# Kernel optimization log

Measured on AMD Instinct MI355X. Metric: run time of the kernel, lower is better.

## Reference

```python
import jax, jax.numpy as jnp
import numpy as np

B, S, H = 1, 2048, 2048
E, I = 16, 1408
I_SHARED = 5632
TOP_K = 2


def setup_inputs() -> dict:
    key = jax.random.key(0)
    ks = jax.random.split(key, 8)
    scale = 0.02
    return {
        "hidden_states": jax.random.normal(ks[0], (B, S, H), dtype=jnp.float32),
        "router_w": jax.random.normal(ks[1], (H, E), dtype=jnp.float32) * scale,
        "expert_gate_up_w": jax.random.normal(ks[2], (E, H, 2 * I), dtype=jnp.float32) * scale,
        "expert_out_w": jax.random.normal(ks[3], (E, I, H), dtype=jnp.float32) * scale,
        "shared_ffw_gate_w": jax.random.normal(ks[4], (H, I_SHARED), dtype=jnp.float32) * scale,
        "shared_ffw_inter_w": jax.random.normal(ks[5], (H, I_SHARED), dtype=jnp.float32) * scale,
        "shared_ffw_out_w": jax.random.normal(ks[6], (I_SHARED, H), dtype=jnp.float32) * scale,
        "shared_gate_w": jax.random.normal(ks[7], (H, 1), dtype=jnp.float32) * scale,
        "top_k": TOP_K,
    }


def reference(hidden_states, router_w, expert_gate_up_w, expert_out_w,
              shared_ffw_gate_w, shared_ffw_inter_w, shared_ffw_out_w,
              shared_gate_w, top_k):
    b, s, h = hidden_states.shape
    e = router_w.shape[-1]
    x = hidden_states.reshape(-1, h)  # [T, H]

    # --- Router: softmax over experts, top-k, renormalize (norm_top_k_prob=True) ---
    router_logits = x @ router_w                        # [T, E]
    router_probs = jax.nn.softmax(router_logits, -1)
    top_p, top_i = jax.lax.top_k(router_probs, top_k)   # [T, K]
    top_p = top_p / jnp.sum(top_p, axis=-1, keepdims=True)
    # dense routing matrix [E, T] (matches one_hot-sum-transpose in source)
    one_hot = jax.nn.one_hot(top_i, e, dtype=top_p.dtype)  # [T, K, E]
    routing_full = jnp.sum(one_hot * top_p[..., None], axis=1).T  # [E, T]

    # --- Dense per-expert SwiGLU over ALL tokens (as in QwenMoeExperts) ---
    gate_up = jnp.einsum('th,ehm->etm', x, expert_gate_up_w)  # [E, T, 2I]
    gate, up = jnp.split(gate_up, 2, axis=-1)
    hidden = up * jax.nn.silu(gate)                           # [E, T, I]
    expert_out = jnp.einsum('eti,eih->eth', hidden, expert_out_w)  # [E, T, H]
    expert_contribution = jnp.einsum('eth,et->th', expert_out, routing_full)

    # --- Shared expert (SwiGLU MLP) with sigmoid gate ---
    sgate = jax.nn.silu(x @ shared_ffw_gate_w)
    sinter = x @ shared_ffw_inter_w
    shared_out = (sinter * sgate) @ shared_ffw_out_w          # [T, H]
    shared_out = shared_out * jax.nn.sigmoid(x @ shared_gate_w)

    out = (expert_contribution + shared_out).reshape(b, s, h)
    return out, router_logits
```

## Files before the change

kernel.cpp:

```cpp
#include <hip/hip_runtime.h>
#include <math.h>

typedef __attribute__((ext_vector_type(4))) float f32x4;
typedef __attribute__((ext_vector_type(2))) unsigned int u32x2;
typedef __attribute__((ext_vector_type(4))) unsigned int u32x4;
typedef __attribute__((ext_vector_type(8))) unsigned short u16x8;
typedef __attribute__((ext_vector_type(8))) __bf16 bf16x8;
typedef unsigned short ushort_t;

#define H_DIM 2048
#define T_TOK 2048
#define NEXP 16
#define I_DIM 1408
#define I2_DIM 2816
#define IS_DIM 5632
#define MAXROWS 6144

static __device__ __forceinline__ unsigned short f2bf(float f){
  union { float f; unsigned u; } v; v.f = f;
  unsigned r = v.u + 0x7FFFu + ((v.u >> 16) & 1u);
  return (unsigned short)(r >> 16);
}
static __device__ __forceinline__ float bf2f(unsigned short h){
  union { unsigned u; float f; } v; v.u = ((unsigned)h) << 16;
  return v.f;
}
static __device__ __forceinline__ float silu_f(float x){ return x / (1.f + __expf(-x)); }

static __device__ __forceinline__ void gld16(const ushort_t* g, ushort_t* l){
  __builtin_amdgcn_global_load_lds(
      (const __attribute__((address_space(1))) unsigned int*)g,
      (__attribute__((address_space(3))) unsigned int*)l, 16, 0, 0);
}
static __device__ __forceinline__ bf16x8 dsr128(unsigned byte_off){
  u32x4 r;
  asm volatile("ds_read_b128 %0, %1" : "=v"(r) : "v"(byte_off));
  return __builtin_bit_cast(bf16x8, r);
}

static __device__ __forceinline__ int swz_r(int nwg, int wgo){
  int q = nwg >> 3, r = nwg & 7;
  int xcd = wgo & 7, idx = wgo >> 3;
  return (xcd < r ? xcd * (q + 1) : r * (q + 1) + (xcd - r) * q) + idx;
}

static __device__ __forceinline__ void tr_tile(const float* __restrict__ in,
                                               ushort_t* __restrict__ out,
                                               int K, int N, int k0, int n0){
  __shared__ float tl[128][65];
  int t = threadIdx.x;
  int lr = t >> 4;
  int lc = t & 15;
  #pragma unroll
  for (int p = 0; p < 8; p++){
    int row = p * 16 + lr;
    f32x4 v = __builtin_nontemporal_load((const f32x4*)&in[(long)(k0 + row) * N + n0 + lc * 4]);
    tl[row][lc*4 + 0] = v[0]; tl[row][lc*4 + 1] = v[1];
    tl[row][lc*4 + 2] = v[2]; tl[row][lc*4 + 3] = v[3];
  }
  __syncthreads();
  #pragma unroll
  for (int p = 0; p < 4; p++){
    int n = p * 16 + lr;
    int kc = lc * 8;
    union { ushort_t s[8]; u32x4 v; } pk;
    #pragma unroll
    for (int j = 0; j < 8; j++) pk.s[j] = f2bf(tl[kc + j][n]);
    __builtin_nontemporal_store(pk.v, (u32x4*)&out[(long)(n0 + n) * K + k0 + kc]);
  }
}

#define TR_O1 11264
#define TR_O2 16896
#define TR_O3 18304
#define TR_O4 19712
#define TR_TOT 21120

__global__ void k_tr_router(const float* __restrict__ x, const float* __restrict__ rw,
                            const float* __restrict__ sgw, float* __restrict__ logits,
                            int* __restrict__ counts, int* __restrict__ lists,
                            float* __restrict__ probs, float* __restrict__ sgmul,
                            ushort_t* __restrict__ xb,
                            const float* __restrict__ wgu, const float* __restrict__ wout,
                            const float* __restrict__ wsg, const float* __restrict__ wsi,
                            const float* __restrict__ wso,
                            ushort_t* __restrict__ wgu_t, ushort_t* __restrict__ wout_t,
                            ushort_t* __restrict__ wsg_t, ushort_t* __restrict__ wsi_t,
                            ushort_t* __restrict__ wso_t){
  int b = blockIdx.x;
  if (b < 512){
    int wid = threadIdx.x >> 6, lane = threadIdx.x & 63;
    int t = b * 4 + wid;
    const float* xr = x + (long)t * H_DIM;
    ushort_t* xbr = xb + (long)t * H_DIM;
    float acc[17];
    #pragma unroll
    for (int e = 0; e < 17; e++) acc[e] = 0.f;
    for (int h0 = lane * 4; h0 < H_DIM; h0 += 256){
      f32x4 xv = *(const f32x4*)&xr[h0];
      u32x2 pk;
      pk[0] = (unsigned)f2bf(xv[0]) | ((unsigned)f2bf(xv[1]) << 16);
      pk[1] = (unsigned)f2bf(xv[2]) | ((unsigned)f2bf(xv[3]) << 16);
      *(u32x2*)&xbr[h0] = pk;
      #pragma unroll
      for (int i = 0; i < 4; i++){
        float xs = xv[i];
        const float* wrow = rw + (long)(h0 + i) * NEXP;
        #pragma unroll
        for (int e = 0; e < 16; e++) acc[e] += xs * wrow[e];
        acc[16] += xs * sgw[h0 + i];
      }
    }
    #pragma unroll
    for (int e = 0; e < 17; e++)
      for (int off = 32; off >= 1; off >>= 1)
        acc[e] += __shfl_xor(acc[e], off);
    if (lane == 0){
      float* lo = logits + (long)t * NEXP;
      #pragma unroll
      for (int e = 0; e < 16; e++) lo[e] = acc[e];
      int e0 = 0;
      #pragma unroll
      for (int e = 1; e < 16; e++) if (acc[e] > acc[e0]) e0 = e;
      int e1 = (e0 == 0) ? 1 : 0;
      #pragma unroll
      for (int e = 0; e < 16; e++) if (e != e0 && acc[e] > acc[e1]) e1 = e;
      float d = acc[e1] - acc[e0];
      float ed = __expf(d);
      float p0 = 1.f / (1.f + ed);
      float p1 = ed / (1.f + ed);
      int pos0 = atomicAdd(&counts[e0], 1);
      lists[e0 * T_TOK + pos0] = t; probs[e0 * T_TOK + pos0] = p0;
      int pos1 = atomicAdd(&counts[e1], 1);
      lists[e1 * T_TOK + pos1] = t; probs[e1 * T_TOK + pos1] = p1;
      sgmul[t] = 1.f / (1.f + __expf(-acc[16]));
    }
    return;
  }
  int bb = b - 512;
  if (bb < TR_O1){
    int e = bb / 704, r = bb % 704;
    int ky = r / 44, nx = r % 44;
    long zo = (long)e * H_DIM * I2_DIM;
    tr_tile(wgu + zo, wgu_t + zo, H_DIM, I2_DIM, ky * 128, nx * 64);
  } else if (bb < TR_O2){
    int r = bb - TR_O1;
    int e = r / 352; r %= 352;
    int ky = r / 32, nx = r % 32;
    long zo = (long)e * I_DIM * H_DIM;
    tr_tile(wout + zo, wout_t + zo, I_DIM, H_DIM, ky * 128, nx * 64);
  } else if (bb < TR_O3){
    int r = bb - TR_O2;
    int ky = r / 88, nx = r % 88;
    tr_tile(wsg, wsg_t, H_DIM, IS_DIM, ky * 128, nx * 64);
  } else if (bb < TR_O4){
    int r = bb - TR_O3;
    int ky = r / 88, nx = r % 88;
    tr_tile(wsi, wsi_t, H_DIM, IS_DIM, ky * 128, nx * 64);
  } else {
    int r = bb - TR_O4;
    int ky = r / 32, nx = r % 32;
    tr_tile(wso, wso_t, IS_DIM, H_DIM, ky * 128, nx * 64);
  }
}

__global__ void bases_k(const int* __restrict__ counts, int* __restrict__ bases){
  if (threadIdx.x == 0){
    int r = 0;
    for (int e = 0; e < NEXP; e++){ bases[e] = r; r += (counts[e] + 127) & ~127; }
  }
}

static __device__ __forceinline__ void gemm_core(
    const ushort_t* __restrict__ Ab, int lda,
    const ushort_t* __restrict__ Bb, int ldbt, int kb,
    int m0, int n0, int cnt, const int* __restrict__ gather, int emode,
    ushort_t* __restrict__ Cb, int ldc, long rbase,
    const int* __restrict__ sclist, const float* __restrict__ scprob,
    const float* __restrict__ svec, float* __restrict__ outp){
  __shared__ ushort_t lds[3 * 8192];
  unsigned lbase = (unsigned)(size_t)(__attribute__((address_space(3))) ushort_t*)lds;

  int tid = threadIdx.x;
  int lane = tid & 63;
  int wv = tid >> 6;
  int wm = wv >> 1;
  int wn = wv & 1;

  int srow = lane >> 2;
  int sslot = ((lane & 3) ^ (srow & 3)) * 8;
  long aoff[2], boff[2];
  #pragma unroll
  for (int c = 0; c < 2; c++){
    int mr = wv * 32 + c * 16 + srow;
    int grow;
    if (gather){
      int j = m0 + mr; if (j >= cnt) j = cnt - 1;
      grow = gather[j];
    } else {
      grow = m0 + mr;
    }
    aoff[c] = (long)grow * lda + sslot;
    boff[c] = (long)(n0 + mr) * ldbt + sslot;
  }

  auto stage = [&](int t, int buf){
    long ko = (long)t * 32;
    ushort_t* dA = lds + buf * 8192 + wv * 1024;
    ushort_t* dB = dA + 4096;
    gld16(Ab + aoff[0] + ko, dA);
    gld16(Ab + aoff[1] + ko, dA + 512);
    gld16(Bb + boff[0] + ko, dB);
    gld16(Bb + boff[1] + ko, dB + 512);
  };

  f32x4 zero = {0.f, 0.f, 0.f, 0.f};
  f32x4 acc[4][4];
  #pragma unroll
  for (int i = 0; i < 4; i++)
    #pragma unroll
    for (int j = 0; j < 4; j++) acc[i][j] = zero;

  int fr = lane & 15;
  int kg = lane >> 4;
  unsigned ps = (unsigned)((kg ^ (fr & 3)) << 4);
  unsigned aoffb = (unsigned)((wm * 64 + fr) * 64) + ps;
  unsigned boffb = 8192u + (unsigned)((wn * 64 + fr) * 64) + ps;

  int nt = kb >> 5;
  stage(0, 0);
  __builtin_amdgcn_sched_barrier(0);
  stage(1, 1);

  int rb = 0, sb = 2;
  for (int t = 0; t < nt; t++){
    if (t + 2 < nt) asm volatile("s_waitcnt vmcnt(4)" ::: "memory");
    else            asm volatile("s_waitcnt vmcnt(0)" ::: "memory");
    __builtin_amdgcn_s_barrier();
    __builtin_amdgcn_sched_barrier(0);
    unsigned bufb = lbase + (unsigned)rb * 16384u;
    bf16x8 af[4], bg[4];
    #pragma unroll
    for (int f = 0; f < 4; f++){
      af[f] = dsr128(bufb + aoffb + f * 1024u);
      bg[f] = dsr128(bufb + boffb + f * 1024u);
    }
    __builtin_amdgcn_sched_barrier(0);
    if (t + 2 < nt) stage(t + 2, sb);
    asm volatile("s_waitcnt lgkmcnt(0)" ::: "memory");
    __builtin_amdgcn_sched_barrier(0);
    #pragma unroll
    for (int fm = 0; fm < 4; fm++)
      #pragma unroll
      for (int fn = 0; fn < 4; fn++)
        acc[fm][fn] = __builtin_amdgcn_mfma_f32_16x16x32_bf16(af[fm], bg[fn], acc[fm][fn], 0, 0, 0);
    rb = (rb == 2) ? 0 : rb + 1;
    sb = (sb == 2) ? 0 : sb + 1;
  }

  int colb = n0 + wn * 64 + (lane & 15);
  int rowb = m0 + wm * 64 + (lane >> 4) * 4;
  #pragma unroll
  for (int fm = 0; fm < 4; fm++){
    #pragma unroll
    for (int fn = 0; fn < 4; fn++){
      f32x4 v = acc[fm][fn];
      int col = colb + fn * 16;
      #pragma unroll
      for (int rr = 0; rr < 4; rr++){
        int m = rowb + fm * 16 + rr;
        if (emode == 0){
          Cb[(long)m * ldc + col] = f2bf(v[rr]);
        } else if (emode == 1){
          if (m < cnt) Cb[(rbase + m) * (long)ldc + col] = f2bf(v[rr]);
        } else if (emode == 2){
          if (m < cnt){
            int tok = sclist[m];
            atomicAdd(outp + (long)tok * ldc + col, scprob[m] * v[rr]);
          }
        } else {
          atomicAdd(outp + (long)m * ldc + col, svec[m] * v[rr]);
        }
      }
    }
  }
}

__global__ __launch_bounds__(256) void g_shared_gi(
    const ushort_t* xb, const ushort_t* wsg_t, const ushort_t* wsi_t, ushort_t* sgr){
  int z = blockIdx.z;
  int wg = swz_r(704, blockIdx.x);
  int m0 = (wg % 16) * 128, n0 = (wg / 16) * 128;
  gemm_core(xb, H_DIM, (z ? wsi_t : wsg_t), H_DIM, H_DIM, m0, n0, T_TOK,
            nullptr, 0, sgr + (size_t)z * T_TOK * IS_DIM, IS_DIM, 0,
            nullptr, nullptr, nullptr, nullptr);
}

__global__ __launch_bounds__(256) void k_gu_flat(
    const ushort_t* xb, const ushort_t* wgu_t, ushort_t* gu,
    const int* counts, const int* bases, const int* lists,
    ushort_t* sg, const ushort_t* si){
  int b = blockIdx.x;
  if (b < 5632){
    int e = b / 352, r = b % 352;
    int wr = swz_r(352, r);
    int m0 = (wr % 16) * 128, n0 = (wr / 16) * 128;
    int cnt = counts[e];
    if (m0 >= cnt) return;
    gemm_core(xb, H_DIM, wgu_t + (size_t)e * I2_DIM * H_DIM, H_DIM, H_DIM,
              m0, n0, cnt, lists + e * T_TOK, 1, gu, I2_DIM, bases[e],
              nullptr, nullptr, nullptr, nullptr);
  } else {
    long i = ((long)(b - 5632) * 256 + threadIdx.x) * 8;
    u16x8 g = *(const u16x8*)&sg[i];
    u16x8 s = *(const u16x8*)&si[i];
    u16x8 o;
    #pragma unroll
    for (int j = 0; j < 8; j++)
      o[j] = f2bf(bf2f(s[j]) * silu_f(bf2f(g[j])));
    *(u16x8*)&sg[i] = o;
  }
}

__global__ __launch_bounds__(256) void k_so_se(
    const ushort_t* sgr, const ushort_t* wso_t, const float* sgmul, float* out,
    const ushort_t* gu, ushort_t* hid){
  int b = blockIdx.x;
  if (b < 1024){
    int kq = b >> 8, r = b & 255;
    int wr = swz_r(256, r);
    int m0 = (wr % 16) * 128, n0 = (wr / 16) * 128;
    gemm_core(sgr + kq * (IS_DIM/4), IS_DIM, wso_t + kq * (IS_DIM/4), IS_DIM, IS_DIM/4,
              m0, n0, T_TOK, nullptr, 3, nullptr, H_DIM, 0,
              nullptr, nullptr, sgmul, out);
  } else {
    long qd = (long)(b - 1024) * 256 + threadIdx.x;
    long r = qd / (I_DIM / 8); int ic = (int)(qd % (I_DIM / 8)) * 8;
    const ushort_t* g = gu + r * I2_DIM + ic;
    u16x8 gv = *(const u16x8*)g;
    u16x8 uv = *(const u16x8*)(g + I_DIM);
    u16x8 ov;
    #pragma unroll
    for (int i = 0; i < 8; i++)
      ov[i] = f2bf(bf2f(uv[i]) * silu_f(bf2f(gv[i])));
    *(u16x8*)&hid[r * I_DIM + ic] = ov;
  }
}

__global__ __launch_bounds__(256) void k_eo(
    const ushort_t* hid, const ushort_t* wout_t,
    const int* counts, const int* bases, const int* lists, const float* probs,
    float* out){
  int b = blockIdx.x;
  int e = b >> 8, r = b & 255;
  int wr = swz_r(256, r);
  int m0 = (wr % 16) * 128, n0 = (wr / 16) * 128;
  int cnt = counts[e];
  if (m0 >= cnt) return;
  gemm_core(hid + (size_t)bases[e] * I_DIM, I_DIM,
            wout_t + (size_t)e * H_DIM * I_DIM, I_DIM, I_DIM,
            m0, n0, cnt, nullptr, 2, nullptr, H_DIM, 0,
            lists + e * T_TOK, probs + e * T_TOK, nullptr, out);
}

extern "C" void kernel_launch(void* const* d_in, const int* in_sizes, int n_in,
                              void* d_out, int out_size, void* d_ws, size_t ws_size,
                              hipStream_t stream){
  const float* x    = (const float*)d_in[0];
  const float* rw   = (const float*)d_in[1];
  const float* wgu  = (const float*)d_in[2];
  const float* wout = (const float*)d_in[3];
  const float* wsg  = (const float*)d_in[4];
  const float* wsi  = (const float*)d_in[5];
  const float* wso  = (const float*)d_in[6];
  const float* sgw  = (const float*)d_in[7];

  float* out = (float*)d_out;
  float* logits = out + (size_t)T_TOK * H_DIM;

  char* w = (char*)d_ws;
  auto alloc = [&](size_t b){ char* p = w; w += (b + 255) & ~(size_t)255; return p; };
  ushort_t* xb     = (ushort_t*)alloc((size_t)T_TOK * H_DIM * 2);
  ushort_t* wgu_t  = (ushort_t*)alloc((size_t)NEXP * I2_DIM * H_DIM * 2);
  ushort_t* wout_t = (ushort_t*)alloc((size_t)NEXP * H_DIM * I_DIM * 2);
  ushort_t* wsg_t  = (ushort_t*)alloc((size_t)IS_DIM * H_DIM * 2);
  ushort_t* wsi_t  = (ushort_t*)alloc((size_t)IS_DIM * H_DIM * 2);
  ushort_t* wso_t  = (ushort_t*)alloc((size_t)H_DIM * IS_DIM * 2);
  ushort_t* sgr    = (ushort_t*)alloc((size_t)2 * T_TOK * IS_DIM * 2);
  ushort_t* sir    = sgr + (size_t)T_TOK * IS_DIM;
  ushort_t* gu     = (ushort_t*)alloc((size_t)MAXROWS * I2_DIM * 2);
  ushort_t* hid    = (ushort_t*)alloc((size_t)MAXROWS * I_DIM * 2);
  int*   counts = (int*)alloc(64);
  int*   bases  = (int*)alloc(64);
  int*   lists  = (int*)alloc((size_t)NEXP * T_TOK * 4);
  float* probs  = (float*)alloc((size_t)NEXP * T_TOK * 4);
  float* sgmul  = (float*)alloc((size_t)T_TOK * 4);

  hipMemsetAsync(counts, 0, 64, stream);
  hipMemsetAsync(out, 0, (size_t)T_TOK * H_DIM * sizeof(float), stream);

  k_tr_router<<<512 + TR_TOT, 256, 0, stream>>>(
      x, rw, sgw, logits, counts, lists, probs, sgmul, xb,
      wgu, wout, wsg, wsi, wso, wgu_t, wout_t, wsg_t, wsi_t, wso_t);
  bases_k<<<1, 64, 0, stream>>>(counts, bases);

  g_shared_gi<<<dim3(704, 1, 2), 256, 0, stream>>>(xb, wsg_t, wsi_t, sgr);

  k_gu_flat<<<5632 + 5632, 256, 0, stream>>>(xb, wgu_t, gu, counts, bases, lists, sgr, sir);

  k_so_se<<<1024 + 4224, 256, 0, stream>>>(sgr, wso_t, sgmul, out, gu, hid);

  k_eo<<<NEXP * 256, 256, 0, stream>>>(hid, wout_t, counts, bases, lists, probs, out);

  (void)in_sizes; (void)n_in; (void)out_size; (void)ws_size;
}
```

Measured before the change: 735.1 us.

## Overlap expert weight transposes with shared-expert GEMM and drop bases kernel

The single transpose-plus-router kernel is split. The shared-expert weights are transposed first, together with the router. The large expert weight transposes then run in the same launch as the shared gate/inter GEMM, so the memory-bound transpose blocks can overlap with the compute-bound GEMM blocks. The bases kernel is removed and each block computes its prefix sum from counts inline. The shared-out split-K factor goes from 4 to 2, halving the atomic adds into out, and nontemporal loads and stores in the transpose are replaced with ordinary ones. In exchange, the merged kernel's LDS size is fixed at 48 KB for every block, which may limit occupancy for the transpose blocks.

```diff
diff --git a/kernel.cpp b/kernel.cpp
--- a/kernel.cpp
+++ b/kernel.cpp
@@ -44,17 +44,23 @@
   return (xcd < r ? xcd * (q + 1) : r * (q + 1) + (xcd - r) * q) + idx;
 }
 
-static __device__ __forceinline__ void tr_tile(const float* __restrict__ in,
+static __device__ __forceinline__ long base_of(const int* __restrict__ counts, int e){
+  long r = 0;
+  for (int i = 0; i < e; i++) r += (counts[i] + 127) & ~127;
+  return r;
+}
+
+static __device__ __forceinline__ void tr_tile(float (*tl)[65],
+                                               const float* __restrict__ in,
                                                ushort_t* __restrict__ out,
                                                int K, int N, int k0, int n0){
-  __shared__ float tl[128][65];
   int t = threadIdx.x;
   int lr = t >> 4;
   int lc = t & 15;
   #pragma unroll
   for (int p = 0; p < 8; p++){
     int row = p * 16 + lr;
-    f32x4 v = __builtin_nontemporal_load((const f32x4*)&in[(long)(k0 + row) * N + n0 + lc * 4]);
+    f32x4 v = *(const f32x4*)&in[(long)(k0 + row) * N + n0 + lc * 4];
     tl[row][lc*4 + 0] = v[0]; tl[row][lc*4 + 1] = v[1];
     tl[row][lc*4 + 2] = v[2]; tl[row][lc*4 + 3] = v[3];
   }
@@ -66,119 +72,18 @@
     union { ushort_t s[8]; u32x4 v; } pk;
     #pragma unroll
     for (int j = 0; j < 8; j++) pk.s[j] = f2bf(tl[kc + j][n]);
-    __builtin_nontemporal_store(pk.v, (u32x4*)&out[(long)(n0 + n) * K + k0 + kc]);
-  }
-}
-
-#define TR_O1 11264
-#define TR_O2 16896
-#define TR_O3 18304
-#define TR_O4 19712
-#define TR_TOT 21120
-
-__global__ void k_tr_router(const float* __restrict__ x, const float* __restrict__ rw,
-                            const float* __restrict__ sgw, float* __restrict__ logits,
-                            int* __restrict__ counts, int* __restrict__ lists,
-                            float* __restrict__ probs, float* __restrict__ sgmul,
-                            ushort_t* __restrict__ xb,
-                            const float* __restrict__ wgu, const float* __restrict__ wout,
-                            const float* __restrict__ wsg, const float* __restrict__ wsi,
-                            const float* __restrict__ wso,
-                            ushort_t* __restrict__ wgu_t, ushort_t* __restrict__ wout_t,
-                            ushort_t* __restrict__ wsg_t, ushort_t* __restrict__ wsi_t,
-                            ushort_t* __restrict__ wso_t){
-  int b = blockIdx.x;
-  if (b < 512){
-    int wid = threadIdx.x >> 6, lane = threadIdx.x & 63;
-    int t = b * 4 + wid;
-    const float* xr = x + (long)t * H_DIM;
-    ushort_t* xbr = xb + (long)t * H_DIM;
-    float acc[17];
-    #pragma unroll
-    for (int e = 0; e < 17; e++) acc[e] = 0.f;
-    for (int h0 = lane * 4; h0 < H_DIM; h0 += 256){
-      f32x4 xv = *(const f32x4*)&xr[h0];
-      u32x2 pk;
-      pk[0] = (unsigned)f2bf(xv[0]) | ((unsigned)f2bf(xv[1]) << 16);
-      pk[1] = (unsigned)f2bf(xv[2]) | ((unsigned)f2bf(xv[3]) << 16);
-      *(u32x2*)&xbr[h0] = pk;
-      #pragma unroll
-      for (int i = 0; i < 4; i++){
-        float xs = xv[i];
-        const float* wrow = rw + (long)(h0 + i) * NEXP;
-        #pragma unroll
-        for (int e = 0; e < 16; e++) acc[e] += xs * wrow[e];
-        acc[16] += xs * sgw[h0 + i];
-      }
-    }
-    #pragma unroll
-    for (int e = 0; e < 17; e++)
-      for (int off = 32; off >= 1; off >>= 1)
-        acc[e] += __shfl_xor(acc[e], off);
-    if (lane == 0){
-      float* lo = logits + (long)t * NEXP;
-      #pragma unroll
-      for (int e = 0; e < 16; e++) lo[e] = acc[e];
-      int e0 = 0;
-      #pragma unroll
-      for (int e = 1; e < 16; e++) if (acc[e] > acc[e0]) e0 = e;
-      int e1 = (e0 == 0) ? 1 : 0;
-      #pragma unroll
-      for (int e = 0; e < 16; e++) if (e != e0 && acc[e] > acc[e1]) e1 = e;
-      float d = acc[e1] - acc[e0];
-      float ed = __expf(d);
-      float p0 = 1.f / (1.f + ed);
-      float p1 = ed / (1.f + ed);
-      int pos0 = atomicAdd(&counts[e0], 1);
-      lists[e0 * T_TOK + pos0] = t; probs[e0 * T_TOK + pos0] = p0;
-      int pos1 = atomicAdd(&counts[e1], 1);
-      lists[e1 * T_TOK + pos1] = t; probs[e1 * T_TOK + pos1] = p1;
-      sgmul[t] = 1.f / (1.f + __expf(-acc[16]));
-    }
-    return;
-  }
-  int bb = b - 512;
-  if (bb < TR_O1){
-    int e = bb / 704, r = bb % 704;
-    int ky = r / 44, nx = r % 44;
-    long zo = (long)e * H_DIM * I2_DIM;
-    tr_tile(wgu + zo, wgu_t + zo, H_DIM, I2_DIM, ky * 128, nx * 64);
-  } else if (bb < TR_O2){
-    int r = bb - TR_O1;
-    int e = r / 352; r %= 352;
-    int ky = r / 32, nx = r % 32;
-    long zo = (long)e * I_DIM * H_DIM;
-    tr_tile(wout + zo, wout_t + zo, I_DIM, H_DIM, ky * 128, nx * 64);
-  } else if (bb < TR_O3){
-    int r = bb - TR_O2;
-    int ky = r / 88, nx = r % 88;
-    tr_tile(wsg, wsg_t, H_DIM, IS_DIM, ky * 128, nx * 64);
-  } else if (bb < TR_O4){
-    int r = bb - TR_O3;
-    int ky = r / 88, nx = r % 88;
-    tr_tile(wsi, wsi_t, H_DIM, IS_DIM, ky * 128, nx * 64);
-  } else {
-    int r = bb - TR_O4;
-    int ky = r / 32, nx = r % 32;
-    tr_tile(wso, wso_t, IS_DIM, H_DIM, ky * 128, nx * 64);
-  }
-}
-
-__global__ void bases_k(const int* __restrict__ counts, int* __restrict__ bases){
-  if (threadIdx.x == 0){
-    int r = 0;
-    for (int e = 0; e < NEXP; e++){ bases[e] = r; r += (counts[e] + 127) & ~127; }
+    *(u32x4*)&out[(long)(n0 + n) * K + k0 + kc] = pk.v;
   }
 }
 
 static __device__ __forceinline__ void gemm_core(
+    ushort_t* __restrict__ lds,
     const ushort_t* __restrict__ Ab, int lda,
     const ushort_t* __restrict__ Bb, int ldbt, int kb,
     int m0, int n0, int cnt, const int* __restrict__ gather, int emode,
     ushort_t* __restrict__ Cb, int ldc, long rbase,
     const int* __restrict__ sclist, const float* __restrict__ scprob,
     const float* __restrict__ svec, float* __restrict__ outp){
-  __shared__ ushort_t lds[3 * 8192];
   unsigned lbase = (unsigned)(size_t)(__attribute__((address_space(3))) ushort_t*)lds;
 
   int tid = threadIdx.x;
@@ -286,29 +191,129 @@
   }
 }
 
-__global__ __launch_bounds__(256) void g_shared_gi(
-    const ushort_t* xb, const ushort_t* wsg_t, const ushort_t* wsi_t, ushort_t* sgr){
-  int z = blockIdx.z;
-  int wg = swz_r(704, blockIdx.x);
-  int m0 = (wg % 16) * 128, n0 = (wg / 16) * 128;
-  gemm_core(xb, H_DIM, (z ? wsi_t : wsg_t), H_DIM, H_DIM, m0, n0, T_TOK,
-            nullptr, 0, sgr + (size_t)z * T_TOK * IS_DIM, IS_DIM, 0,
-            nullptr, nullptr, nullptr, nullptr);
+__global__ void k_tr1(const float* __restrict__ x, const float* __restrict__ rw,
+                      const float* __restrict__ sgw, float* __restrict__ logits,
+                      int* __restrict__ counts, int* __restrict__ lists,
+                      float* __restrict__ probs, float* __restrict__ sgmul,
+                      ushort_t* __restrict__ xb,
+                      const float* __restrict__ wsg, const float* __restrict__ wsi,
+                      const float* __restrict__ wso,
+                      ushort_t* __restrict__ wsg_t, ushort_t* __restrict__ wsi_t,
+                      ushort_t* __restrict__ wso_t){
+  __shared__ float tl[128][65];
+  int b = blockIdx.x;
+  if (b < 512){
+    int wid = threadIdx.x >> 6, lane = threadIdx.x & 63;
+    int t = b * 4 + wid;
+    const float* xr = x + (long)t * H_DIM;
+    ushort_t* xbr = xb + (long)t * H_DIM;
+    float acc[17];
+    #pragma unroll
+    for (int e = 0; e < 17; e++) acc[e] = 0.f;
+    for (int h0 = lane * 4; h0 < H_DIM; h0 += 256){
+      f32x4 xv = *(const f32x4*)&xr[h0];
+      u32x2 pk;
+      pk[0] = (unsigned)f2bf(xv[0]) | ((unsigned)f2bf(xv[1]) << 16);
+      pk[1] = (unsigned)f2bf(xv[2]) | ((unsigned)f2bf(xv[3]) << 16);
+      *(u32x2*)&xbr[h0] = pk;
+      #pragma unroll
+      for (int i = 0; i < 4; i++){
+        float xs = xv[i];
+        const float* wrow = rw + (long)(h0 + i) * NEXP;
+        #pragma unroll
+        for (int e = 0; e < 16; e++) acc[e] += xs * wrow[e];
+        acc[16] += xs * sgw[h0 + i];
+      }
+    }
+    #pragma unroll
+    for (int e = 0; e < 17; e++)
+      for (int off = 32; off >= 1; off >>= 1)
+        acc[e] += __shfl_xor(acc[e], off);
+    if (lane == 0){
+      float* lo = logits + (long)t * NEXP;
+      #pragma unroll
+      for (int e = 0; e < 16; e++) lo[e] = acc[e];
+      int e0 = 0;
+      #pragma unroll
+      for (int e = 1; e < 16; e++) if (acc[e] > acc[e0]) e0 = e;
+      int e1 = (e0 == 0) ? 1 : 0;
+      #pragma unroll
+      for (int e = 0; e < 16; e++) if (e != e0 && acc[e] > acc[e1]) e1 = e;
+      float d = acc[e1] - acc[e0];
+      float ed = __expf(d);
+      float p0 = 1.f / (1.f + ed);
+      float p1 = ed / (1.f + ed);
+      int pos0 = atomicAdd(&counts[e0], 1);
+      lists[e0 * T_TOK + pos0] = t; probs[e0 * T_TOK + pos0] = p0;
+      int pos1 = atomicAdd(&counts[e1], 1);
+      lists[e1 * T_TOK + pos1] = t; probs[e1 * T_TOK + pos1] = p1;
+      sgmul[t] = 1.f / (1.f + __expf(-acc[16]));
+    }
+    return;
+  }
+  int bb = b - 512;
+  if (bb < 1408){
+    int ky = bb / 88, nx = bb % 88;
+    tr_tile(tl, wsg, wsg_t, H_DIM, IS_DIM, ky * 128, nx * 64);
+  } else if (bb < 2816){
+    int r = bb - 1408;
+    int ky = r / 88, nx = r % 88;
+    tr_tile(tl, wsi, wsi_t, H_DIM, IS_DIM, ky * 128, nx * 64);
+  } else {
+    int r = bb - 2816;
+    int ky = r / 32, nx = r % 32;
+    tr_tile(tl, wso, wso_t, IS_DIM, H_DIM, ky * 128, nx * 64);
+  }
+}
+
+__global__ __launch_bounds__(256) void k_gi_tr2(
+    const ushort_t* __restrict__ xb, const ushort_t* __restrict__ wsg_t,
+    const ushort_t* __restrict__ wsi_t, ushort_t* __restrict__ sgr,
+    const float* __restrict__ wgu, const float* __restrict__ wout,
+    ushort_t* __restrict__ wgu_t, ushort_t* __restrict__ wout_t){
+  __shared__ char smem[49152];
+  int b = blockIdx.x;
+  if (b < 1408){
+    int z = b & 1;
+    int wg = swz_r(704, b >> 1);
+    int m0 = (wg % 16) * 128, n0 = (wg / 16) * 128;
+    gemm_core((ushort_t*)smem, xb, H_DIM, (z ? wsi_t : wsg_t), H_DIM, H_DIM,
+              m0, n0, T_TOK, nullptr, 0,
+              sgr + (size_t)z * T_TOK * IS_DIM, IS_DIM, 0,
+              nullptr, nullptr, nullptr, nullptr);
+    return;
+  }
+  float (*tl)[65] = (float(*)[65])smem;
+  int bb = b - 1408;
+  if (bb < 11264){
+    int e = bb / 704, r = bb % 704;
+    int ky = r / 44, nx = r % 44;
+    long zo = (long)e * H_DIM * I2_DIM;
+    tr_tile(tl, wgu + zo, wgu_t + zo, H_DIM, I2_DIM, ky * 128, nx * 64);
+  } else {
+    int r = bb - 11264;
+    int e = r / 352; r %= 352;
+    int ky = r / 32, nx = r % 32;
+    long zo = (long)e * I_DIM * H_DIM;
+    tr_tile(tl, wout + zo, wout_t + zo, I_DIM, H_DIM, ky * 128, nx * 64);
+  }
 }
 
 __global__ __launch_bounds__(256) void k_gu_flat(
-    const ushort_t* xb, const ushort_t* wgu_t, ushort_t* gu,
-    const int* counts, const int* bases, const int* lists,
-    ushort_t* sg, const ushort_t* si){
+    const ushort_t* __restrict__ xb, const ushort_t* __restrict__ wgu_t,
+    ushort_t* __restrict__ gu,
+    const int* __restrict__ counts, const int* __restrict__ lists,
+    ushort_t* __restrict__ sg, const ushort_t* __restrict__ si){
   int b = blockIdx.x;
   if (b < 5632){
+    __shared__ ushort_t lds[3 * 8192];
     int e = b / 352, r = b % 352;
     int wr = swz_r(352, r);
     int m0 = (wr % 16) * 128, n0 = (wr / 16) * 128;
     int cnt = counts[e];
     if (m0 >= cnt) return;
-    gemm_core(xb, H_DIM, wgu_t + (size_t)e * I2_DIM * H_DIM, H_DIM, H_DIM,
-              m0, n0, cnt, lists + e * T_TOK, 1, gu, I2_DIM, bases[e],
+    gemm_core(lds, xb, H_DIM, wgu_t + (size_t)e * I2_DIM * H_DIM, H_DIM, H_DIM,
+              m0, n0, cnt, lists + e * T_TOK, 1, gu, I2_DIM, base_of(counts, e),
               nullptr, nullptr, nullptr, nullptr);
   } else {
     long i = ((long)(b - 5632) * 256 + threadIdx.x) * 8;
@@ -323,18 +328,20 @@
 }
 
 __global__ __launch_bounds__(256) void k_so_se(
-    const ushort_t* sgr, const ushort_t* wso_t, const float* sgmul, float* out,
-    const ushort_t* gu, ushort_t* hid){
+    const ushort_t* __restrict__ sgr, const ushort_t* __restrict__ wso_t,
+    const float* __restrict__ sgmul, float* __restrict__ out,
+    const ushort_t* __restrict__ gu, ushort_t* __restrict__ hid){
   int b = blockIdx.x;
-  if (b < 1024){
+  if (b < 512){
+    __shared__ ushort_t lds[3 * 8192];
     int kq = b >> 8, r = b & 255;
     int wr = swz_r(256, r);
     int m0 = (wr % 16) * 128, n0 = (wr / 16) * 128;
-    gemm_core(sgr + kq * (IS_DIM/4), IS_DIM, wso_t + kq * (IS_DIM/4), IS_DIM, IS_DIM/4,
+    gemm_core(lds, sgr + kq * (IS_DIM/2), IS_DIM, wso_t + kq * (IS_DIM/2), IS_DIM, IS_DIM/2,
               m0, n0, T_TOK, nullptr, 3, nullptr, H_DIM, 0,
               nullptr, nullptr, sgmul, out);
   } else {
-    long qd = (long)(b - 1024) * 256 + threadIdx.x;
+    long qd = (long)(b - 512) * 256 + threadIdx.x;
     long r = qd / (I_DIM / 8); int ic = (int)(qd % (I_DIM / 8)) * 8;
     const ushort_t* g = gu + r * I2_DIM + ic;
     u16x8 gv = *(const u16x8*)g;
@@ -348,16 +355,17 @@
 }
 
 __global__ __launch_bounds__(256) void k_eo(
-    const ushort_t* hid, const ushort_t* wout_t,
-    const int* counts, const int* bases, const int* lists, const float* probs,
-    float* out){
+    const ushort_t* __restrict__ hid, const ushort_t* __restrict__ wout_t,
+    const int* __restrict__ counts, const int* __restrict__ lists,
+    const float* __restrict__ probs, float* __restrict__ out){
+  __shared__ ushort_t lds[3 * 8192];
   int b = blockIdx.x;
   int e = b >> 8, r = b & 255;
   int wr = swz_r(256, r);
   int m0 = (wr % 16) * 128, n0 = (wr / 16) * 128;
   int cnt = counts[e];
   if (m0 >= cnt) return;
-  gemm_core(hid + (size_t)bases[e] * I_DIM, I_DIM,
+  gemm_core(lds, hid + (size_t)base_of(counts, e) * I_DIM, I_DIM,
             wout_t + (size_t)e * H_DIM * I_DIM, I_DIM, I_DIM,
             m0, n0, cnt, nullptr, 2, nullptr, H_DIM, 0,
             lists + e * T_TOK, probs + e * T_TOK, nullptr, out);
@@ -391,7 +399,6 @@
   ushort_t* gu     = (ushort_t*)alloc((size_t)MAXROWS * I2_DIM * 2);
   ushort_t* hid    = (ushort_t*)alloc((size_t)MAXROWS * I_DIM * 2);
   int*   counts = (int*)alloc(64);
-  int*   bases  = (int*)alloc(64);
   int*   lists  = (int*)alloc((size_t)NEXP * T_TOK * 4);
   float* probs  = (float*)alloc((size_t)NEXP * T_TOK * 4);
   float* sgmul  = (float*)alloc((size_t)T_TOK * 4);
@@ -399,18 +406,13 @@
   hipMemsetAsync(counts, 0, 64, stream);
   hipMemsetAsync(out, 0, (size_t)T_TOK * H_DIM * sizeof(float), stream);
 
-  k_tr_router<<<512 + TR_TOT, 256, 0, stream>>>(
-      x, rw, sgw, logits, counts, lists, probs, sgmul, xb,
-      wgu, wout, wsg, wsi, wso, wgu_t, wout_t, wsg_t, wsi_t, wso_t);
-  bases_k<<<1, 64, 0, stream>>>(counts, bases);
-
-  g_shared_gi<<<dim3(704, 1, 2), 256, 0, stream>>>(xb, wsg_t, wsi_t, sgr);
-
-  k_gu_flat<<<5632 + 5632, 256, 0, stream>>>(xb, wgu_t, gu, counts, bases, lists, sgr, sir);
-
-  k_so_se<<<1024 + 4224, 256, 0, stream>>>(sgr, wso_t, sgmul, out, gu, hid);
-
-  k_eo<<<NEXP * 256, 256, 0, stream>>>(hid, wout_t, counts, bases, lists, probs, out);
+  k_tr1<<<4736, 256, 0, stream>>>(x, rw, sgw, logits, counts, lists, probs, sgmul, xb,
+                                  wsg, wsi, wso, wsg_t, wsi_t, wso_t);
+  k_gi_tr2<<<1408 + 16896, 256, 0, stream>>>(xb, wsg_t, wsi_t, sgr,
+                                             wgu, wout, wgu_t, wout_t);
+  k_gu_flat<<<5632 + 5632, 256, 0, stream>>>(xb, wgu_t, gu, counts, lists, sgr, sir);
+  k_so_se<<<512 + 4224, 256, 0, stream>>>(sgr, wso_t, sgmul, out, gu, hid);
+  k_eo<<<NEXP * 256, 256, 0, stream>>>(hid, wout_t, counts, lists, probs, out);
 
   (void)in_sizes; (void)n_in; (void)out_size; (void)ws_size;
 }
```

After: 707.9 us (median of 3 runs). 1.04x faster.
